# Kernel tuning notes

Hardware: AMD Instinct MI355X
Metric: run time of the kernel (lower is better)

Reference implementation:

```python
import jax, jax.numpy as jnp
import numpy as np

EPS = 1e-06

def knn(k_pos, q_pos, k):
    # k_pos: (B,N,3), q_pos: (B,S,3) -> idx (B,S,k) of nearest points in k_pos
    # squared euclidean distances (B,S,N)
    d2 = (jnp.sum(q_pos**2, -1)[:, :, None]
          - 2.0 * jnp.einsum('bsc,bnc->bsn', q_pos, k_pos)
          + jnp.sum(k_pos**2, -1)[:, None, :])
    _, idx = jax.lax.top_k(-d2, k)
    return idx

def linear(x, W, b):
    # torch nn.Linear: y = x @ W.T + b, W: (out,in)
    return jnp.einsum('...i,oi->...o', x, W) + b

def setup_inputs() -> dict:
    key = jax.random.key(0)
    ks = jax.random.split(key, 12)
    B, S, N, D = 4, 1024, 16384, 128
    sc = 1.0 / np.sqrt(D)
    inp = {
        'q_feat': jax.random.normal(ks[0], (B, S, D), jnp.float32),
        'k_feat': jax.random.normal(ks[1], (B, N, D), jnp.float32),
        'q_pos': jax.random.uniform(ks[2], (B, S, 3), jnp.float32),
        'k_pos': jax.random.uniform(ks[3], (B, N, 3), jnp.float32),
        'Wq': jax.random.normal(ks[4], (D, D), jnp.float32) * sc,
        'bq': jnp.zeros((D,), jnp.float32),
        'Wk': jax.random.normal(ks[5], (D, D), jnp.float32) * sc,
        'bk': jnp.zeros((D,), jnp.float32),
        'Wv': jax.random.normal(ks[6], (D, D), jnp.float32) * sc,
        'bv': jnp.zeros((D,), jnp.float32),
        'W1': jax.random.normal(ks[7], (D, 3), jnp.float32) * (1.0 / np.sqrt(3.0)),
        'b1': jnp.zeros((D,), jnp.float32),
        'W2': jax.random.normal(ks[8], (D, D), jnp.float32) * sc,
        'b2': jnp.zeros((D,), jnp.float32),
    }
    return inp

def reference(q_feat, k_feat, q_pos, k_pos, Wq, bq, Wk, bk, Wv, bv, W1, b1, W2, b2):
    KNN_K = 16
    q = linear(q_feat, Wq, bq)          # (B,S,D)
    k = linear(k_feat, Wk, bk)          # (B,N,D)
    v = linear(k_feat, Wv, bv)          # (B,N,D)
    idx = knn(k_pos, q_pos, KNN_K)      # (B,S,k)
    # gather neighbors: (B,S,k,D) and (B,S,k,3)
    k_nb = jnp.take_along_axis(k[:, None, :, :], idx[..., None], axis=2)
    v_nb = jnp.take_along_axis(v[:, None, :, :], idx[..., None], axis=2)
    kpos_nb = jnp.take_along_axis(k_pos[:, None, :, :], idx[..., None], axis=2)
    rel_pos = q_pos[:, :, None, :] - kpos_nb                     # (B,S,k,3)
    pe = linear(jax.nn.relu(linear(rel_pos, W1, b1)), W2, b2)    # (B,S,k,D)
    scores = jnp.sum(q[:, :, None, :] - k_nb + pe, axis=-1)      # (B,S,k)
    attn = jax.nn.softmax(scores, axis=-1)                       # softmax over k
    attn = attn / (jnp.sum(attn, axis=1, keepdims=True) + EPS)   # normalize over S
    out = jnp.sum(attn[..., None] * v_nb, axis=2)                # (B,S,D)
    return out
```

## Files before the change

kernel.cpp:

```cpp
#include <hip/hip_runtime.h>
#include <hip/hip_bf16.h>

#define BB 4
#define SS 1024
#define NPTS 16384
#define DD 128
#define EPSF 1e-6f

#define OFF_W2S    256
#define OFF_SCL    384
#define OFF_COL    448
#define OFF_QSUM   512
#define OFF_KSUM   4608
#define OFF_IDX    70144
#define OFF_ATTN   135680
#define OFF_G      205312
#define OFF_WVT    729600

__device__ __forceinline__ unsigned long long shflxor_u64(unsigned long long v, int m) {
  unsigned int lo = (unsigned int)(v & 0xffffffffull);
  unsigned int hi = (unsigned int)(v >> 32);
  lo = (unsigned int)__shfl_xor((int)lo, m, 64);
  hi = (unsigned int)__shfl_xor((int)hi, m, 64);
  return ((unsigned long long)hi << 32) | (unsigned long long)lo;
}

__device__ __forceinline__ unsigned long long u64min(unsigned long long a, unsigned long long b) {
  return a < b ? a : b;
}

__device__ __forceinline__ unsigned long long wavemin_u64(unsigned long long v) {
#pragma unroll
  for (int m = 1; m <= 32; m <<= 1) v = u64min(v, shflxor_u64(v, m));
  return v;
}

__global__ __launch_bounds__(256) void k_pre(const float* __restrict__ kf,
                                             const float* __restrict__ qf,
                                             const float* __restrict__ kpos,
                                             const float* __restrict__ Wq,
                                             const float* __restrict__ bq,
                                             const float* __restrict__ Wk,
                                             const float* __restrict__ bk,
                                             const float* __restrict__ Wv,
                                             const float* __restrict__ W2,
                                             const float* __restrict__ b2,
                                             float* __restrict__ ws) {
  const int tid = threadIdx.x;
  const int bid = (int)blockIdx.x;
  __shared__ __align__(16) float cq_s[128];
  __shared__ __align__(16) float ck_s[128];
  __shared__ float part[256];
  __shared__ float scl_s[2];

  {
    const int j = tid & 127, h = tid >> 7;
    const int r0 = h * 64;
    float sq = 0.f, sk = 0.f;
    for (int r = r0; r < r0 + 64; ++r) {
      sq += Wq[r * DD + j];
      sk += Wk[r * DD + j];
    }
    part[tid] = sq;
    __syncthreads();
    if (h == 0) cq_s[j] = part[j] + part[128 + j];
    __syncthreads();
    part[tid] = sk;
    __syncthreads();
    if (h == 0) ck_s[j] = part[j] + part[128 + j];
  }
  if (tid < 64) {
    float a0 = bq[tid] + bq[tid + 64];
    float a1 = bk[tid] + bk[tid + 64];
#pragma unroll
    for (int m = 1; m <= 32; m <<= 1) {
      a0 += __shfl_xor(a0, m, 64);
      a1 += __shfl_xor(a1, m, 64);
    }
    if (tid == 0) { scl_s[0] = a0; scl_s[1] = a1; }
  }

  if (bid < 128) {
    if (tid < 128) ws[OFF_WVT + bid * DD + tid] = Wv[tid * DD + bid];
  } else if (bid == 128) {
    if (tid < 64) ws[OFF_COL + tid] = 0.f;
  } else if (bid == 256) {
    const int j = tid & 127, h = tid >> 7;
    const int r0 = h * 64;
    float s2 = 0.f;
    for (int r = r0; r < r0 + 64; ++r) s2 += W2[r * DD + j];
    __syncthreads();
    part[tid] = s2;
    __syncthreads();
    if (h == 0) ws[OFF_W2S + j] = part[j] + part[128 + j];
    if (tid < 64) {
      float a2 = b2[tid] + b2[tid + 64];
#pragma unroll
      for (int m = 1; m <= 32; m <<= 1) a2 += __shfl_xor(a2, m, 64);
      if (tid == 0) ws[OFF_SCL + 2] = a2;
    }
  }

  const int pid = bid * 256 + tid;
  if (pid < BB * NPTS) {
    const float x = kpos[pid * 3 + 0], y = kpos[pid * 3 + 1], z = kpos[pid * 3 + 2];
    const float kk = __fadd_rn(__fadd_rn(__fmul_rn(x, x), __fmul_rn(y, y)), __fmul_rn(z, z));
    ((float4*)(ws + OFF_G))[pid] = make_float4(x, y, z, kk);
  }
  __syncthreads();
  const float bqs = scl_s[0], bks = scl_s[1];

  const int g = (bid * 256 + tid) >> 4;
  const int gl = tid & 15;
  const int ngroups = (int)gridDim.x * 16;
  const int total = BB * NPTS + BB * SS;
  for (int row = g; row < total; row += ngroups) {
    const float* x;
    const float* c;
    if (row < BB * NPTS) { x = kf + (size_t)row * DD; c = ck_s; }
    else                 { x = qf + (size_t)(row - BB * NPTS) * DD; c = cq_s; }
    float4 a  = *(const float4*)(x + gl * 4);
    float4 b  = *(const float4*)(x + 64 + gl * 4);
    float4 ca = *(const float4*)(c + gl * 4);
    float4 cb = *(const float4*)(c + 64 + gl * 4);
    float s = a.x * ca.x + a.y * ca.y + a.z * ca.z + a.w * ca.w
            + b.x * cb.x + b.y * cb.y + b.z * cb.z + b.w * cb.w;
    s += __shfl_xor(s, 1, 64);
    s += __shfl_xor(s, 2, 64);
    s += __shfl_xor(s, 4, 64);
    s += __shfl_xor(s, 8, 64);
    if (gl == 0) {
      if (row < BB * NPTS) ws[OFF_KSUM + row] = s + bks;
      else                 ws[OFF_QSUM + (row - BB * NPTS)] = s + bqs;
    }
  }
}

#define FORQ(X) X(0) X(1) X(2) X(3) X(4) X(5) X(6) X(7)

__global__ __launch_bounds__(512, 6) void k_knn(const float* __restrict__ qpos,
                                                const float* __restrict__ kpos,
                                                const float* __restrict__ W1,
                                                const float* __restrict__ b1,
                                                float* __restrict__ ws) {
  __shared__ unsigned long long cbuf[8][8][48];
  __shared__ float pmins[8][8][64];
  __shared__ int cnts[8][8];
  const int tid = threadIdx.x;
  const int w = tid >> 6, l = tid & 63;
  const int qbase = (int)blockIdx.x * 8;
  const int b = qbase >> 10;

  const float4* kp4 = (const float4*)(ws + OFF_G) + (size_t)b * NPTS;
  const float* kp = kpos + (size_t)b * NPTS * 3;

#define LOADQ(i) \
  const float qx##i = qpos[(size_t)(qbase + i) * 3 + 0]; \
  const float qy##i = qpos[(size_t)(qbase + i) * 3 + 1]; \
  const float qz##i = qpos[(size_t)(qbase + i) * 3 + 2]; \
  const float qq##i = __fadd_rn(__fadd_rn(__fmul_rn(qx##i, qx##i), __fmul_rn(qy##i, qy##i)), __fmul_rn(qz##i, qz##i));
  FORQ(LOADQ)
#undef LOADQ

  const int sbase = w * 2048;

#define DECLMN(i) float mn##i = 3.4e38f;
  FORQ(DECLMN)
#undef DECLMN
  {
    const float4* p0 = kp4 + sbase + l;
    float4 c0 = p0[0], c1 = p0[64], c2 = p0[128], c3 = p0[192];
    const float4* nx = p0 + 256;
#define P1Q(i, cc) { \
      const float dA = fmaf(qx##i, (cc).x, fmaf(qy##i, (cc).y, __fmul_rn(qz##i, (cc).z))); \
      const float sF = fmaf(-2.0f, dA, (cc).w); \
      mn##i = fminf(mn##i, sF); }
#define P1_PT(cc, RELOAD) { \
      P1Q(0, cc) P1Q(1, cc) P1Q(2, cc) P1Q(3, cc) \
      P1Q(4, cc) P1Q(5, cc) P1Q(6, cc) P1Q(7, cc) \
      cc = RELOAD; }
    for (int t = 0; t < 8; ++t) {
      P1_PT(c0, nx[0])
      P1_PT(c1, nx[64])
      P1_PT(c2, nx[128])
      P1_PT(c3, nx[192])
      nx += 256;
    }
#undef P1_PT
  }
#define STMN(i) pmins[w][i][l] = mn##i;
  FORQ(STMN)
#undef STMN
  __syncthreads();

#define CUTQ(i) float cut##i; { \
    float m = pmins[0][i][l]; \
    m = fminf(m, pmins[1][i][l]); m = fminf(m, pmins[2][i][l]); \
    m = fminf(m, pmins[3][i][l]); m = fminf(m, pmins[4][i][l]); \
    m = fminf(m, pmins[5][i][l]); m = fminf(m, pmins[6][i][l]); \
    m = fminf(m, pmins[7][i][l]); \
    m = fminf(m, __shfl_xor(m, 16, 64)); \
    m = fminf(m, __shfl_xor(m, 32, 64)); \
    m = fmaxf(m, __shfl_xor(m, 1, 64)); \
    m = fmaxf(m, __shfl_xor(m, 2, 64)); \
    m = fmaxf(m, __shfl_xor(m, 4, 64)); \
    m = fmaxf(m, __shfl_xor(m, 8, 64)); \
    cut##i = m + 2e-5f; }
  FORQ(CUTQ)
#undef CUTQ

#define DECLCNT(i) int cnt##i = 0;
  FORQ(DECLCNT)
#undef DECLCNT
  {
    const float4* p0 = kp4 + sbase + l;
    float4 c0 = p0[0], c1 = p0[64], c2 = p0[128], c3 = p0[192];
    const float4* nx = p0 + 256;
    int p = sbase + l;
#define P2Q(i, cc, pp) { \
      const float dA = fmaf(qx##i, (cc).x, fmaf(qy##i, (cc).y, __fmul_rn(qz##i, (cc).z))); \
      const float sF = fmaf(-2.0f, dA, (cc).w); \
      const bool pred = (sF <= cut##i); \
      const unsigned long long mask = __ballot(pred); \
      if (mask) { \
        if (pred) { \
          const float dotE = __fadd_rn(__fadd_rn(__fmul_rn(qz##i, (cc).z), __fmul_rn(qy##i, (cc).y)), __fmul_rn(qx##i, (cc).x)); \
          const float d2e = __fadd_rn(__fsub_rn(qq##i, __fmul_rn(2.0f, dotE)), (cc).w); \
          unsigned int u = __float_as_uint(d2e); \
          u ^= (unsigned int)((int)u >> 31) | 0x80000000u; \
          const int off = __builtin_amdgcn_mbcnt_hi((unsigned int)(mask >> 32), \
                          __builtin_amdgcn_mbcnt_lo((unsigned int)mask, 0)); \
          const int pos = cnt##i + off; \
          if (pos < 48) cbuf[i][w][pos] = ((unsigned long long)u << 32) | (unsigned int)(pp); \
        } \
        cnt##i += (int)__popcll(mask); \
      } }
#define P2_PT(cc, RELOAD, POFF) { \
      P2Q(0, cc, p + POFF) P2Q(1, cc, p + POFF) P2Q(2, cc, p + POFF) P2Q(3, cc, p + POFF) \
      P2Q(4, cc, p + POFF) P2Q(5, cc, p + POFF) P2Q(6, cc, p + POFF) P2Q(7, cc, p + POFF) \
      cc = RELOAD; }
    for (int t = 0; t < 8; ++t) {
      P2_PT(c0, nx[0], 0)
      P2_PT(c1, nx[64], 64)
      P2_PT(c2, nx[128], 128)
      P2_PT(c3, nx[192], 192)
      nx += 256;
      p += 256;
    }
#undef P2_PT
#undef P2Q
  }
#define STCNT(i) if (l == 0) cnts[i][w] = (cnt##i > 48 ? 48 : cnt##i);
  FORQ(STCNT)
#undef STCNT
  __syncthreads();

  const int qi = w;
  const int q = qbase + qi;
  unsigned long long cand[8];
#pragma unroll
  for (int i = 0; i < 8; ++i) {
    const int cn = cnts[qi][i];
    cand[i] = (l < cn) ? cbuf[qi][i][l] : ~0ull;
  }
  unsigned long long lmin = cand[0]; int lpos = 0;
#pragma unroll
  for (int i = 1; i < 8; ++i) { if (cand[i] < lmin) { lmin = cand[i]; lpos = i; } }
  unsigned long long sel64 = 0;
  for (int r = 0; r < 16; ++r) {
    const unsigned long long m = wavemin_u64(lmin);
    if (l == r) sel64 = m;
    if (lmin == m) {
#pragma unroll
      for (int i = 0; i < 8; ++i) cand[i] = (lpos == i) ? ~0ull : cand[i];
      lmin = cand[0]; lpos = 0;
#pragma unroll
      for (int i = 1; i < 8; ++i) { if (cand[i] < lmin) { lmin = cand[i]; lpos = i; } }
    }
  }
  const int myidx = (int)(sel64 & 0xffffffffull);
  if (l < 16) ((int*)(ws + OFF_IDX))[q * 16 + l] = myidx;

  const float* qpw = qpos + (size_t)q * 3;
  const float gx = qpw[0], gy = qpw[1], gz = qpw[2];
  const int j = l & 15;
  const int pj = __shfl(myidx, j, 64);
  const float* kpj = kp + (size_t)pj * 3;
  const float rx = gx - kpj[0];
  const float ry = gy - kpj[1];
  const float rz = gz - kpj[2];
  float pe = 0.f;
  const int i0 = (l >> 4) * 32;
  for (int i = i0; i < i0 + 32; ++i) {
    float hh = fmaf(rx, W1[i * 3 + 0], fmaf(ry, W1[i * 3 + 1], fmaf(rz, W1[i * 3 + 2], b1[i])));
    hh = fmaxf(hh, 0.f);
    pe = fmaf(hh, ws[OFF_W2S + i], pe);
  }
  pe += __shfl_xor(pe, 16, 64);
  pe += __shfl_xor(pe, 32, 64);
  float score = ws[OFF_QSUM + q] - ws[OFF_KSUM + b * NPTS + pj] + pe + ws[OFF_SCL + 2];
  float mx = score;
  mx = fmaxf(mx, __shfl_xor(mx, 1, 64));
  mx = fmaxf(mx, __shfl_xor(mx, 2, 64));
  mx = fmaxf(mx, __shfl_xor(mx, 4, 64));
  mx = fmaxf(mx, __shfl_xor(mx, 8, 64));
  const float e = expf(score - mx);
  float se = e;
  se += __shfl_xor(se, 1, 64);
  se += __shfl_xor(se, 2, 64);
  se += __shfl_xor(se, 4, 64);
  se += __shfl_xor(se, 8, 64);
  const float attn = e / se;
  if (l < 16) {
    ws[OFF_ATTN + q * 16 + l] = attn;
    atomicAdd(&ws[OFF_COL + b * 16 + l], attn);
  }
}

__global__ __launch_bounds__(256) void k_go(const float* __restrict__ kf,
                                            const float* __restrict__ bv,
                                            const float* __restrict__ ws,
                                            float* __restrict__ out) {
  __shared__ float xg[8 * 128];
  __shared__ float as_s[8];
  const int tid = threadIdx.x;
  const int w = tid >> 6, l = tid & 63;
  const int qbase = (int)blockIdx.x * 8;
  const int b = qbase >> 10;
  const float* kb = kf + (size_t)b * NPTS * DD;

#pragma unroll
  for (int u = 0; u < 2; ++u) {
    const int qi = w * 2 + u;
    const int q = qbase + qi;
    float a = 0.f;
    int pidx = 0;
    if (l < 16) {
      a = ws[OFF_ATTN + q * 16 + l] / (ws[OFF_COL + b * 16 + l] + EPSF);
      pidx = ((const int*)(ws + OFF_IDX))[q * 16 + l];
    }
    float asum = a;
    asum += __shfl_xor(asum, 1, 64);
    asum += __shfl_xor(asum, 2, 64);
    asum += __shfl_xor(asum, 4, 64);
    asum += __shfl_xor(asum, 8, 64);
    if (l == 0) as_s[qi] = asum;
    float acc0 = 0.f, acc1 = 0.f;
#pragma unroll
    for (int jj = 0; jj < 16; ++jj) {
      const float aj = __shfl(a, jj, 64);
      const int pj = __shfl(pidx, jj, 64);
      const float* row = kb + (size_t)pj * DD;
      acc0 = fmaf(aj, row[l], acc0);
      acc1 = fmaf(aj, row[64 + l], acc1);
    }
    xg[qi * 128 + l] = acc0;
    xg[qi * 128 + 64 + l] = acc1;
  }
  __syncthreads();

  const int o = tid & 127, rg = tid >> 7;
  const float bvo = bv[o];
  float acc[4];
#pragma unroll
  for (int r = 0; r < 4; ++r) acc[r] = as_s[rg * 4 + r] * bvo;
  for (int i = 0; i < DD; ++i) {
    const float wv = ws[OFF_WVT + i * DD + o];
#pragma unroll
    for (int r = 0; r < 4; ++r) acc[r] = fmaf(wv, xg[(rg * 4 + r) * 128 + i], acc[r]);
  }
#pragma unroll
  for (int r = 0; r < 4; ++r) out[(size_t)(qbase + rg * 4 + r) * DD + o] = acc[r];
}

extern "C" void kernel_launch(void* const* d_in, const int* in_sizes, int n_in,
                              void* d_out, int out_size, void* d_ws, size_t ws_size,
                              hipStream_t stream) {
  const float* qf   = (const float*)d_in[0];
  const float* kf   = (const float*)d_in[1];
  const float* qpos = (const float*)d_in[2];
  const float* kpos = (const float*)d_in[3];
  const float* Wq   = (const float*)d_in[4];
  const float* bq   = (const float*)d_in[5];
  const float* Wk   = (const float*)d_in[6];
  const float* bk   = (const float*)d_in[7];
  const float* Wv   = (const float*)d_in[8];
  const float* bv   = (const float*)d_in[9];
  const float* W1   = (const float*)d_in[10];
  const float* b1   = (const float*)d_in[11];
  const float* W2   = (const float*)d_in[12];
  const float* b2   = (const float*)d_in[13];
  float* ws  = (float*)d_ws;
  float* out = (float*)d_out;

  k_pre<<<1024, 256, 0, stream>>>(kf, qf, kpos, Wq, bq, Wk, bk, Wv, W2, b2, ws);
  k_knn<<<512, 512, 0, stream>>>(qpos, kpos, W1, b1, ws);
  k_go<<<512, 256, 0, stream>>>(kf, bv, ws, out);
}
```

Measured before the change: 175.3 us.

## Compute k/q row sums lazily in knn kernel, only for selected neighbors

Stops precomputing the key row-sum for all B*N points (32 MB of k_feat reads) in the pre-kernel. Each knn block now builds the column sums of Wq, Wk and W2 in shared memory, computes its query sum directly, and computes key sums only for the 16 selected neighbours of each query. The pre-kernel shrinks to 256 blocks. In exchange every knn block redundantly reduces three 128x128 weight matrices, which adds extra syncs and shared memory and may lower occupancy. The per-neighbour gathers of k_feat rows are scattered reads.

```diff
diff --git a/kernel.cpp b/kernel.cpp
--- a/kernel.cpp
+++ b/kernel.cpp
@@ -7,11 +7,7 @@
 #define DD 128
 #define EPSF 1e-6f
 
-#define OFF_W2S    256
-#define OFF_SCL    384
 #define OFF_COL    448
-#define OFF_QSUM   512
-#define OFF_KSUM   4608
 #define OFF_IDX    70144
 #define OFF_ATTN   135680
 #define OFF_G      205312
@@ -35,121 +31,97 @@
   return v;
 }
 
-__global__ __launch_bounds__(256) void k_pre(const float* __restrict__ kf,
-                                             const float* __restrict__ qf,
-                                             const float* __restrict__ kpos,
-                                             const float* __restrict__ Wq,
-                                             const float* __restrict__ bq,
-                                             const float* __restrict__ Wk,
-                                             const float* __restrict__ bk,
+__global__ __launch_bounds__(256) void k_pre(const float* __restrict__ kpos,
                                              const float* __restrict__ Wv,
-                                             const float* __restrict__ W2,
-                                             const float* __restrict__ b2,
                                              float* __restrict__ ws) {
   const int tid = threadIdx.x;
   const int bid = (int)blockIdx.x;
-  __shared__ __align__(16) float cq_s[128];
-  __shared__ __align__(16) float ck_s[128];
-  __shared__ float part[256];
-  __shared__ float scl_s[2];
-
-  {
-    const int j = tid & 127, h = tid >> 7;
-    const int r0 = h * 64;
-    float sq = 0.f, sk = 0.f;
-    for (int r = r0; r < r0 + 64; ++r) {
-      sq += Wq[r * DD + j];
-      sk += Wk[r * DD + j];
-    }
-    part[tid] = sq;
-    __syncthreads();
-    if (h == 0) cq_s[j] = part[j] + part[128 + j];
-    __syncthreads();
-    part[tid] = sk;
-    __syncthreads();
-    if (h == 0) ck_s[j] = part[j] + part[128 + j];
-  }
-  if (tid < 64) {
-    float a0 = bq[tid] + bq[tid + 64];
-    float a1 = bk[tid] + bk[tid + 64];
-#pragma unroll
-    for (int m = 1; m <= 32; m <<= 1) {
-      a0 += __shfl_xor(a0, m, 64);
-      a1 += __shfl_xor(a1, m, 64);
-    }
-    if (tid == 0) { scl_s[0] = a0; scl_s[1] = a1; }
-  }
-
   if (bid < 128) {
     if (tid < 128) ws[OFF_WVT + bid * DD + tid] = Wv[tid * DD + bid];
   } else if (bid == 128) {
     if (tid < 64) ws[OFF_COL + tid] = 0.f;
-  } else if (bid == 256) {
-    const int j = tid & 127, h = tid >> 7;
-    const int r0 = h * 64;
-    float s2 = 0.f;
-    for (int r = r0; r < r0 + 64; ++r) s2 += W2[r * DD + j];
-    __syncthreads();
-    part[tid] = s2;
-    __syncthreads();
-    if (h == 0) ws[OFF_W2S + j] = part[j] + part[128 + j];
-    if (tid < 64) {
-      float a2 = b2[tid] + b2[tid + 64];
-#pragma unroll
-      for (int m = 1; m <= 32; m <<= 1) a2 += __shfl_xor(a2, m, 64);
-      if (tid == 0) ws[OFF_SCL + 2] = a2;
-    }
-  }
-
+  }
   const int pid = bid * 256 + tid;
   if (pid < BB * NPTS) {
     const float x = kpos[pid * 3 + 0], y = kpos[pid * 3 + 1], z = kpos[pid * 3 + 2];
     const float kk = __fadd_rn(__fadd_rn(__fmul_rn(x, x), __fmul_rn(y, y)), __fmul_rn(z, z));
     ((float4*)(ws + OFF_G))[pid] = make_float4(x, y, z, kk);
   }
-  __syncthreads();
-  const float bqs = scl_s[0], bks = scl_s[1];
-
-  const int g = (bid * 256 + tid) >> 4;
-  const int gl = tid & 15;
-  const int ngroups = (int)gridDim.x * 16;
-  const int total = BB * NPTS + BB * SS;
-  for (int row = g; row < total; row += ngroups) {
-    const float* x;
-    const float* c;
-    if (row < BB * NPTS) { x = kf + (size_t)row * DD; c = ck_s; }
-    else                 { x = qf + (size_t)(row - BB * NPTS) * DD; c = cq_s; }
-    float4 a  = *(const float4*)(x + gl * 4);
-    float4 b  = *(const float4*)(x + 64 + gl * 4);
-    float4 ca = *(const float4*)(c + gl * 4);
-    float4 cb = *(const float4*)(c + 64 + gl * 4);
-    float s = a.x * ca.x + a.y * ca.y + a.z * ca.z + a.w * ca.w
-            + b.x * cb.x + b.y * cb.y + b.z * cb.z + b.w * cb.w;
-    s += __shfl_xor(s, 1, 64);
-    s += __shfl_xor(s, 2, 64);
-    s += __shfl_xor(s, 4, 64);
-    s += __shfl_xor(s, 8, 64);
-    if (gl == 0) {
-      if (row < BB * NPTS) ws[OFF_KSUM + row] = s + bks;
-      else                 ws[OFF_QSUM + (row - BB * NPTS)] = s + bqs;
-    }
-  }
 }
 
 #define FORQ(X) X(0) X(1) X(2) X(3) X(4) X(5) X(6) X(7)
 
-__global__ __launch_bounds__(512, 6) void k_knn(const float* __restrict__ qpos,
+__global__ __launch_bounds__(512, 6) void k_knn(const float* __restrict__ qf,
+                                                const float* __restrict__ kf,
+                                                const float* __restrict__ qpos,
                                                 const float* __restrict__ kpos,
+                                                const float* __restrict__ Wq,
+                                                const float* __restrict__ bq,
+                                                const float* __restrict__ Wk,
+                                                const float* __restrict__ bk,
                                                 const float* __restrict__ W1,
                                                 const float* __restrict__ b1,
+                                                const float* __restrict__ W2,
+                                                const float* __restrict__ b2,
                                                 float* __restrict__ ws) {
   __shared__ unsigned long long cbuf[8][8][48];
   __shared__ float pmins[8][8][64];
   __shared__ int cnts[8][8];
+  __shared__ __align__(16) float cq_s[128];
+  __shared__ __align__(16) float ck_s[128];
+  __shared__ __align__(16) float w2s_s[128];
+  __shared__ float part[256];
+  __shared__ float scl_s[3];
   const int tid = threadIdx.x;
   const int w = tid >> 6, l = tid & 63;
   const int qbase = (int)blockIdx.x * 8;
   const int b = qbase >> 10;
+
+  {
+    float sq = 0.f, sk = 0.f, s2 = 0.f;
+    const int jj = tid & 127, hh = (tid >> 7) & 1;
+    if (tid < 256) {
+      const int r0 = hh * 64;
+      for (int r = r0; r < r0 + 64; ++r) {
+        sq += Wq[r * DD + jj];
+        sk += Wk[r * DD + jj];
+        s2 += W2[r * DD + jj];
+      }
+    }
+    if (tid < 256) part[tid] = sq;
+    __syncthreads();
+    if (tid < 128) cq_s[tid] = part[tid] + part[128 + tid];
+    __syncthreads();
+    if (tid < 256) part[tid] = sk;
+    __syncthreads();
+    if (tid < 128) ck_s[tid] = part[tid] + part[128 + tid];
+    __syncthreads();
+    if (tid < 256) part[tid] = s2;
+    __syncthreads();
+    if (tid < 128) w2s_s[tid] = part[tid] + part[128 + tid];
+    if (tid < 64) {
+      float a0 = bq[tid] + bq[tid + 64];
+      float a1 = bk[tid] + bk[tid + 64];
+      float a2 = b2[tid] + b2[tid + 64];
+#pragma unroll
+      for (int m = 1; m <= 32; m <<= 1) {
+        a0 += __shfl_xor(a0, m, 64);
+        a1 += __shfl_xor(a1, m, 64);
+        a2 += __shfl_xor(a2, m, 64);
+      }
+      if (tid == 0) { scl_s[0] = a0; scl_s[1] = a1; scl_s[2] = a2; }
+    }
+    __syncthreads();
+  }
+
+  float qsum_w;
+  {
+    const float* qrow = qf + (size_t)(qbase + w) * DD;
+    float s = fmaf(qrow[l + 64], cq_s[l + 64], __fmul_rn(qrow[l], cq_s[l]));
+#pragma unroll
+    for (int m = 1; m <= 32; m <<= 1) s += __shfl_xor(s, m, 64);
+    qsum_w = s + scl_s[0];
+  }
 
   const float4* kp4 = (const float4*)(ws + OFF_G) + (size_t)b * NPTS;
   const float* kp = kpos + (size_t)b * NPTS * 3;
@@ -289,16 +261,32 @@
   const float rx = gx - kpj[0];
   const float ry = gy - kpj[1];
   const float rz = gz - kpj[2];
+  const int i0 = (l >> 4) * 32;
   float pe = 0.f;
-  const int i0 = (l >> 4) * 32;
   for (int i = i0; i < i0 + 32; ++i) {
     float hh = fmaf(rx, W1[i * 3 + 0], fmaf(ry, W1[i * 3 + 1], fmaf(rz, W1[i * 3 + 2], b1[i])));
     hh = fmaxf(hh, 0.f);
-    pe = fmaf(hh, ws[OFF_W2S + i], pe);
+    pe = fmaf(hh, w2s_s[i], pe);
+  }
+  float ks = 0.f;
+  {
+    const float4* k4 = (const float4*)(kf + (size_t)b * NPTS * DD + (size_t)pj * DD + i0);
+    const float4* c4 = (const float4*)(ck_s + i0);
+#pragma unroll
+    for (int ii = 0; ii < 8; ++ii) {
+      const float4 kv = k4[ii];
+      const float4 cv = c4[ii];
+      ks = fmaf(kv.x, cv.x, ks);
+      ks = fmaf(kv.y, cv.y, ks);
+      ks = fmaf(kv.z, cv.z, ks);
+      ks = fmaf(kv.w, cv.w, ks);
+    }
   }
   pe += __shfl_xor(pe, 16, 64);
   pe += __shfl_xor(pe, 32, 64);
-  float score = ws[OFF_QSUM + q] - ws[OFF_KSUM + b * NPTS + pj] + pe + ws[OFF_SCL + 2];
+  ks += __shfl_xor(ks, 16, 64);
+  ks += __shfl_xor(ks, 32, 64);
+  float score = qsum_w - (ks + scl_s[1]) + pe + scl_s[2];
   float mx = score;
   mx = fmaxf(mx, __shfl_xor(mx, 1, 64));
   mx = fmaxf(mx, __shfl_xor(mx, 2, 64));
@@ -393,7 +381,7 @@
   float* ws  = (float*)d_ws;
   float* out = (float*)d_out;
 
-  k_pre<<<1024, 256, 0, stream>>>(kf, qf, kpos, Wq, bq, Wk, bk, Wv, W2, b2, ws);
-  k_knn<<<512, 512, 0, stream>>>(qpos, kpos, W1, b1, ws);
+  k_pre<<<256, 256, 0, stream>>>(kpos, Wv, ws);
+  k_knn<<<512, 512, 0, stream>>>(qf, kf, qpos, kpos, Wq, bq, Wk, bk, W1, b1, W2, b2, ws);
   k_go<<<512, 256, 0, stream>>>(kf, bv, ws, out);
 }
```

New measurement: 186.6 us. 6.4% more time.
